# Kernel optimization log

Hardware: AMD Instinct MI355X
Metric: run time of the kernel (lower is better)

The kernel has to match this reference:

```python
import jax, jax.numpy as jnp
import numpy as np

B, T, E, NH, VOCAB, MULT = 1, 1024, 768, 12, 32000, 32
N = E * MULT // NH  # 2048
LN_EPS = 1e-5


def setup_inputs() -> dict:
    key = jax.random.key(0)
    ks = jax.random.split(key, 6)
    return {
        "idx": jax.random.randint(ks[0], (B, T), 0, VOCAB),
        "embed": jax.random.normal(ks[1], (VOCAB, E), jnp.float32) * 0.02,
        "encoder": jax.random.normal(ks[2], (NH, E, N), jnp.float32) * 0.02,
        "encoder_v": jax.random.normal(ks[3], (NH, E, N), jnp.float32) * 0.02,
        "decoder": jax.random.normal(ks[4], (NH * N, E), jnp.float32) * 0.02,
        "lm_head": jax.random.normal(ks[5], (VOCAB, E), jnp.float32) * 0.02,
        "ln_w": jnp.ones((E,), jnp.float32),
        "ln_b": jnp.zeros((E,), jnp.float32),
        "n_layer": 6,
    }


def reference(idx, embed, encoder, encoder_v, decoder, lm_head, ln_w, ln_b, n_layer):
    nh, e, n = encoder.shape
    t = idx.shape[1]
    dec = decoder.reshape(nh, n, e)  # flatten order (h, n) -> h*N + n

    def ln(x):
        m = jnp.mean(x, axis=-1, keepdims=True)
        v = jnp.mean(jnp.square(x - m), axis=-1, keepdims=True)
        return (x - m) * jax.lax.rsqrt(v + LN_EPS) * ln_w + ln_b

    causal = jnp.tril(jnp.ones((t, t), bool))  # [T, T]
    scale = 1.0 / np.sqrt(n).astype(np.float32)

    x = ln(embed[idx])  # [B, T, E]  (the unsqueezed head dim broadcasts; keep it squeezed)
    for _ in range(n_layer):
        # encoder projection + ReLU: [B,T,E] x [H,E,N] -> [B,H,T,N]
        x_sparse = jax.nn.relu(jnp.einsum("bte,hen->bhtn", x, encoder))
        # hand-rolled causal attention, Q=K=x_sparse, V=x (broadcast over heads)
        scores = jnp.einsum("bhqn,bhkn->bhqk", x_sparse, x_sparse) * scale
        scores = jnp.where(causal, scores, -jnp.inf)
        attn = jax.nn.softmax(scores, axis=-1)
        y = jnp.einsum("bhqk,bke->bhqe", attn, x)  # [B,H,T,E]
        y = ln(y)
        y_sparse = jax.nn.relu(jnp.einsum("bhte,hen->bhtn", y, encoder_v))
        xy = x_sparse * y_sparse  # [B,H,T,N]; dropout p=0 -> identity
        y_mlp = jnp.einsum("bhtn,hne->bte", xy, dec)  # decoder matmul
        x = ln(x + ln(y_mlp))
    logits = jnp.einsum("bte,ve->btv", x, lm_head)
    return logits
```

## Files before the change

kernel.cpp:

```cpp
#include <hip/hip_runtime.h>

typedef unsigned short u16;
typedef short bf16x8 __attribute__((ext_vector_type(8)));
typedef float f32x4 __attribute__((ext_vector_type(4)));
typedef u16 u16x4 __attribute__((ext_vector_type(4)));

#define TT     1024
#define EE     768
#define NHH    12
#define ND     2048
#define VOC    32000
#define HNN    24576
#define NLAYER 6
#define LN_EPS 1e-5f

__device__ __forceinline__ float b2f(u16 u){
  unsigned int x = ((unsigned int)u) << 16; float f; __builtin_memcpy(&f, &x, 4); return f;
}
__device__ __forceinline__ u16 f2b(float f){
  unsigned int x; __builtin_memcpy(&x, &f, 4);
  x = x + 0x7fffu + ((x >> 16) & 1u);
  return (u16)(x >> 16);
}

__device__ __forceinline__ void gload16(const void* g, void* lds){
  __builtin_amdgcn_global_load_lds(
      (const __attribute__((address_space(1))) unsigned int*)g,
      (__attribute__((address_space(3))) unsigned int*)(unsigned int)(unsigned long long)lds,
      16, 0, 0);
}

__device__ __forceinline__ bf16x8 ldsr(unsigned addr){
  bf16x8 r;
  asm volatile("ds_read_b128 %0, %1" : "=v"(r) : "v"(addr));
  return r;
}

__device__ __forceinline__ void blk_sum2(float& a, float& b){
  #pragma unroll
  for (int o = 32; o > 0; o >>= 1){ a += __shfl_down(a, o); b += __shfl_down(b, o); }
  __shared__ float sa[4], sb[4];
  int lane = threadIdx.x & 63, wid = threadIdx.x >> 6;
  __syncthreads();
  if (lane == 0){ sa[wid] = a; sb[wid] = b; }
  __syncthreads();
  a = (sa[0] + sa[1]) + (sa[2] + sa[3]);
  b = (sb[0] + sb[1]) + (sb[2] + sb[3]);
}
__device__ __forceinline__ float blk_max(float v){
  #pragma unroll
  for (int o = 32; o > 0; o >>= 1) v = fmaxf(v, __shfl_down(v, o));
  __shared__ float sm[4];
  int lane = threadIdx.x & 63, wid = threadIdx.x >> 6;
  __syncthreads();
  if (lane == 0) sm[wid] = v;
  __syncthreads();
  return fmaxf(fmaxf(sm[0], sm[1]), fmaxf(sm[2], sm[3]));
}
__device__ __forceinline__ float blk_sum(float v){
  #pragma unroll
  for (int o = 32; o > 0; o >>= 1) v += __shfl_down(v, o);
  __shared__ float ss[4];
  int lane = threadIdx.x & 63, wid = threadIdx.x >> 6;
  __syncthreads();
  if (lane == 0) ss[wid] = v;
  __syncthreads();
  return (ss[0] + ss[1]) + (ss[2] + ss[3]);
}

__global__ void transpose_f2b(const float* __restrict__ in, long sIn,
                              u16* __restrict__ out, long sOut, int R, int Cc){
  __shared__ float tile[32][33];
  int z = blockIdx.z;
  in  += (long)z * sIn;
  out += (long)z * sOut;
  int c0 = blockIdx.x * 32, r0 = blockIdx.y * 32;
  int lx = threadIdx.x & 31, ly = threadIdx.x >> 5;
  #pragma unroll
  for (int i = 0; i < 32; i += 8)
    tile[ly + i][lx] = in[(long)(r0 + ly + i) * Cc + (c0 + lx)];
  __syncthreads();
  #pragma unroll
  for (int i = 0; i < 32; i += 8)
    out[(long)(c0 + ly + i) * R + (r0 + lx)] = f2b(tile[lx][ly + i]);
}

__global__ void conv_f2b(const float* __restrict__ in, u16* __restrict__ out){
  long i = ((long)blockIdx.x * 256 + threadIdx.x) * 4;
  float4 v = *(const float4*)(in + i);
  u16x4 o; o.x = f2b(v.x); o.y = f2b(v.y); o.z = f2b(v.z); o.w = f2b(v.w);
  *(u16x4*)(out + i) = o;
}

__global__ void embed_ln(const int* __restrict__ idx, const float* __restrict__ emb,
                         const float* __restrict__ w, const float* __restrict__ b,
                         float* __restrict__ xf, u16* __restrict__ xb, u16* __restrict__ xT){
  int t = blockIdx.x, tid = threadIdx.x;
  const float* src = emb + (long)idx[t] * EE;
  float v[3];
  #pragma unroll
  for (int j = 0; j < 3; j++) v[j] = src[tid + j * 256];
  float s = v[0] + v[1] + v[2];
  float s2 = v[0]*v[0] + v[1]*v[1] + v[2]*v[2];
  blk_sum2(s, s2);
  float m  = s * (1.0f / EE);
  float var = s2 * (1.0f / EE) - m * m;
  float rs = rsqrtf(var + LN_EPS);
  #pragma unroll
  for (int j = 0; j < 3; j++){
    int e = tid + j * 256;
    float o = (v[j] - m) * rs * w[e] + b[e];
    xf[(long)t * EE + e] = o;
    u16 ob = f2b(o);
    xb[(long)t * EE + e] = ob;
    xT[(long)e * TT + t] = ob;
  }
}

__global__ void ln_rows(const float* __restrict__ in, u16* __restrict__ out,
                        const float* __restrict__ w, const float* __restrict__ b){
  long row = blockIdx.x; int tid = threadIdx.x;
  const float* src = in + row * EE;
  float v[3];
  #pragma unroll
  for (int j = 0; j < 3; j++) v[j] = src[tid + j * 256];
  float s = v[0] + v[1] + v[2];
  float s2 = v[0]*v[0] + v[1]*v[1] + v[2]*v[2];
  blk_sum2(s, s2);
  float m = s * (1.0f / EE);
  float var = s2 * (1.0f / EE) - m * m;
  float rs = rsqrtf(var + LN_EPS);
  #pragma unroll
  for (int j = 0; j < 3; j++){
    int e = tid + j * 256;
    out[row * EE + e] = f2b((v[j] - m) * rs * w[e] + b[e]);
  }
}

__global__ void softmax_rows(const float* __restrict__ scores, u16* __restrict__ attn){
  int q = blockIdx.x, h = blockIdx.y, tid = threadIdx.x;
  const float* srow = scores + ((long)h * TT + q) * TT;
  u16* arow = attn + ((long)h * TT + q) * TT;
  float4 v = *(const float4*)(srow + tid * 4);
  float mx = blk_max(fmaxf(fmaxf(v.x, v.y), fmaxf(v.z, v.w)));
  float e0 = __expf(v.x - mx), e1 = __expf(v.y - mx);
  float e2 = __expf(v.z - mx), e3 = __expf(v.w - mx);
  float inv = 1.0f / blk_sum(e0 + e1 + e2 + e3);
  u16x4 o; o.x = f2b(e0 * inv); o.y = f2b(e1 * inv); o.z = f2b(e2 * inv); o.w = f2b(e3 * inv);
  *(u16x4*)(arow + tid * 4) = o;
}

__global__ void residual_ln(const float* __restrict__ part, const float* __restrict__ xin,
                            float* __restrict__ xf, u16* __restrict__ xb, u16* __restrict__ xT,
                            const float* __restrict__ w, const float* __restrict__ b){
  int t = blockIdx.x, tid = threadIdx.x;
  float g[3];
  #pragma unroll
  for (int j = 0; j < 3; j++){
    int e = tid + j * 256;
    float s = 0.f;
    #pragma unroll
    for (int pp = 0; pp < 8; pp++) s += part[((long)pp * TT + t) * EE + e];
    g[j] = s;
  }
  float s = g[0] + g[1] + g[2], s2 = g[0]*g[0] + g[1]*g[1] + g[2]*g[2];
  blk_sum2(s, s2);
  float m = s * (1.0f / EE), var = s2 * (1.0f / EE) - m * m;
  float rs = rsqrtf(var + LN_EPS);
  float hh[3];
  #pragma unroll
  for (int j = 0; j < 3; j++){
    int e = tid + j * 256;
    hh[j] = xin[(long)t * EE + e] + ((g[j] - m) * rs * w[e] + b[e]);
  }
  s = hh[0] + hh[1] + hh[2]; s2 = hh[0]*hh[0] + hh[1]*hh[1] + hh[2]*hh[2];
  blk_sum2(s, s2);
  m = s * (1.0f / EE); var = s2 * (1.0f / EE) - m * m; rs = rsqrtf(var + LN_EPS);
  #pragma unroll
  for (int j = 0; j < 3; j++){
    int e = tid + j * 256;
    float o = (hh[j] - m) * rs * w[e] + b[e];
    xf[(long)t * EE + e] = o;
    u16 ob = f2b(o);
    xb[(long)t * EE + e] = ob;
    xT[(long)e * TT + t] = ob;
  }
}

template<int BM, int BN, int WM, int WN, int DEPTH, int EPI>
__global__ __launch_bounds__(WM*WN*64, 2)
void gemm_pipe(const u16* __restrict__ Ab, long sA,
               const u16* __restrict__ Bb, long sB,
               void* __restrict__ Cb, long sC,
               int grid_m, int grid_mn,
               int K, int lda, int ldb, int ldc, float scale,
               const u16* __restrict__ Mul, long sMul, int ldmul){
  constexpr int THREADS = WM*WN*64;
  constexpr int WMR = BM/WM, WNR = BN/WN;
  constexpr int MI = WMR/16, NI = WNR/16;
  constexpr int BUF  = (BM+BN)*32;
  constexpr int BUFB = BUF*2;
  constexpr int NBUF = DEPTH+1;
  constexpr int AIT = (BM*4)/THREADS, BIT = (BN*4)/THREADS;
  __shared__ __align__(16) u16 S[NBUF*BUF];

  const int nwg = gridDim.x;
  const int orig = blockIdx.x;
  const int q = nwg >> 3, r = nwg & 7;
  const int xcd = orig & 7;
  const int wgid = (xcd < r ? xcd*(q+1) : r*(q+1) + (xcd - r)*q) + (orig >> 3);
  const int z   = wgid / grid_mn;
  const int rem = wgid - z*grid_mn;
  const int nb  = rem / grid_m;
  const int mb  = rem - nb*grid_m;
  const int m0 = mb*BM, n0 = nb*BN;
  const int tid = threadIdx.x, lane = tid & 63, wid = tid >> 6;

  if (EPI == 2 && n0 > m0 + (BM - 1)){
    float* C = (float*)Cb + (long)z * sC;
    constexpr int FIT = (BM*BN)/(THREADS*4);
    #pragma unroll
    for (int i = 0; i < FIT; i++){
      int idx4 = (tid + i*THREADS)*4;
      int rr = idx4 / BN, cc = idx4 - rr*BN;
      *(float4*)&C[(long)(m0+rr)*ldc + n0 + cc] = make_float4(-1e30f,-1e30f,-1e30f,-1e30f);
    }
    return;
  }

  const u16* A = Ab + (long)z*sA;
  const u16* B = Bb + (long)z*sB;

  const int rS = tid >> 2;
  const int cS = (((tid & 3) ^ ((rS >> 1) & 3)) << 3);
  const u16* gA[AIT]; const u16* gB[BIT];
  #pragma unroll
  for (int i = 0; i < AIT; i++) gA[i] = A + (long)(m0 + rS + i*(THREADS/4))*lda + cS;
  #pragma unroll
  for (int i = 0; i < BIT; i++) gB[i] = B + (long)(n0 + rS + i*(THREADS/4))*ldb + cS;

  auto stage = [&](int kt, int buf){
    const int tb = buf*BUF;
    const int ko = kt << 5;
    #pragma unroll
    for (int i = 0; i < AIT; i++)
      gload16(gA[i] + ko, (void*)&S[tb + (i*THREADS + wid*64)*8]);
    #pragma unroll
    for (int i = 0; i < BIT; i++)
      gload16(gB[i] + ko, (void*)&S[tb + BM*32 + (i*THREADS + wid*64)*8]);
  };

  const int wr = wid / WN, wc = wid - wr*WN;
  const int fr = lane & 15, fk = lane >> 4;
  const unsigned ldsBase = (unsigned)(unsigned long long)&S[0];
  unsigned aAd[MI], bAd[NI];
  #pragma unroll
  for (int mi = 0; mi < MI; mi++){
    int rowm = wr*WMR + mi*16 + fr;
    aAd[mi] = ldsBase + (unsigned)(rowm*32 + ((fk ^ ((rowm >> 1) & 3)) << 3)) * 2u;
  }
  #pragma unroll
  for (int ni = 0; ni < NI; ni++){
    int rown = wc*WNR + ni*16 + fr;
    bAd[ni] = ldsBase + (unsigned)(BM*32 + rown*32 + ((fk ^ ((rown >> 1) & 3)) << 3)) * 2u;
  }

  f32x4 acc[MI][NI] = {};

  #pragma unroll
  for (int d = 0; d < DEPTH; d++) stage(d, d);
  if constexpr (DEPTH == 3) asm volatile("s_waitcnt vmcnt(8)" ::: "memory");
  else                      asm volatile("s_waitcnt vmcnt(4)" ::: "memory");
  __builtin_amdgcn_s_barrier();
  __builtin_amdgcn_sched_barrier(0);

  const int NT = K >> 5;
  int rb = 0, wb = DEPTH % NBUF;
  for (int t = 0; t < NT; t++){
    int nx = t + DEPTH; nx = nx < NT ? nx : NT - 1;
    stage(nx, wb);
    const unsigned rbB = (unsigned)rb * BUFB;
    bf16x8 bfr[NI], afr[MI];
    #pragma unroll
    for (int ni = 0; ni < NI; ni++) bfr[ni] = ldsr(bAd[ni] + rbB);
    #pragma unroll
    for (int mi = 0; mi < MI; mi++) afr[mi] = ldsr(aAd[mi] + rbB);
    asm volatile("s_waitcnt lgkmcnt(0)" ::: "memory");
    __builtin_amdgcn_sched_barrier(0);
    __builtin_amdgcn_s_setprio(1);
    #pragma unroll
    for (int mi = 0; mi < MI; mi++)
      #pragma unroll
      for (int ni = 0; ni < NI; ni++)
        acc[mi][ni] = __builtin_amdgcn_mfma_f32_16x16x32_bf16(afr[mi], bfr[ni], acc[mi][ni], 0, 0, 0);
    __builtin_amdgcn_s_setprio(0);
    __builtin_amdgcn_sched_barrier(0);
    if constexpr (DEPTH == 3) asm volatile("s_waitcnt vmcnt(8)" ::: "memory");
    else                      asm volatile("s_waitcnt vmcnt(4)" ::: "memory");
    __builtin_amdgcn_s_barrier();
    __builtin_amdgcn_sched_barrier(0);
    rb = (rb + 1 == NBUF) ? 0 : rb + 1;
    wb = (wb + 1 == NBUF) ? 0 : wb + 1;
  }

  const int er = (lane >> 4) * 4, ec = lane & 15;
  #pragma unroll
  for (int mi = 0; mi < MI; mi++){
    #pragma unroll
    for (int ni = 0; ni < NI; ni++){
      #pragma unroll
      for (int j = 0; j < 4; j++){
        int row = m0 + wr*WMR + mi*16 + er + j;
        int col = n0 + wc*WNR + ni*16 + ec;
        float v = acc[mi][ni][j];
        if (EPI == 0){
          ((float*)Cb + (long)z * sC)[(long)row * ldc + col] = v;
        } else if (EPI == 1){
          v = v > 0.f ? v : 0.f;
          ((u16*)Cb + (long)z * sC)[(long)row * ldc + col] = f2b(v);
        } else if (EPI == 2){
          v *= scale;
          if (col > row) v = -1e30f;
          ((float*)Cb + (long)z * sC)[(long)row * ldc + col] = v;
        } else {
          v = v > 0.f ? v : 0.f;
          float mfv = b2f((Mul + (long)z * sMul)[(long)row * ldmul + col]);
          ((u16*)Cb + (long)z * sC)[(long)row * ldc + col] = f2b(v * mfv);
        }
      }
    }
  }
  asm volatile("s_waitcnt vmcnt(0)" ::: "memory");
}

extern "C" void kernel_launch(void* const* d_in, const int* in_sizes, int n_in,
                              void* d_out, int out_size, void* d_ws, size_t ws_size,
                              hipStream_t stream){
  (void)in_sizes; (void)n_in; (void)out_size; (void)ws_size;
  const int*   idx     = (const int*)  d_in[0];
  const float* embed   = (const float*)d_in[1];
  const float* encoder = (const float*)d_in[2];
  const float* encv    = (const float*)d_in[3];
  const float* decoder = (const float*)d_in[4];
  const float* lm_head = (const float*)d_in[5];
  const float* ln_w    = (const float*)d_in[6];
  const float* ln_b    = (const float*)d_in[7];
  float* out = (float*)d_out;

  char* p = (char*)d_ws;
  auto take = [&](size_t n){ char* r = p; p += (n + 255) & ~(size_t)255; return r; };
  u16*   encT  = (u16*)  take((size_t)NHH * ND * EE * 2);
  u16*   encvT = (u16*)  take((size_t)NHH * ND * EE * 2);
  u16*   decT  = (u16*)  take((size_t)EE * HNN * 2);
  u16*   lmhB  = (u16*)  take((size_t)VOC * EE * 2);
  float* xf    = (float*)take((size_t)TT * EE * 4);
  u16*   xb    = (u16*)  take((size_t)TT * EE * 2);
  u16*   xT    = (u16*)  take((size_t)EE * TT * 2);
  u16*   xs    = (u16*)  take((size_t)NHH * TT * ND * 2);
  char*  big   =         take((size_t)NHH * TT * TT * 4);
  u16*   attn  = (u16*)  take((size_t)NHH * TT * TT * 2);
  u16*   yb    = (u16*)  take((size_t)NHH * TT * EE * 2);
  float* part  = (float*)take((size_t)8 * TT * EE * 4);
  float* scores = (float*)big;
  float* yf     = (float*)big;
  u16*   xy     = (u16*)big;

  dim3 blk(256, 1, 1);

  transpose_f2b<<<dim3(ND / 32, EE / 32, NHH), blk, 0, stream>>>(encoder, (long)EE * ND, encT,  (long)ND * EE, EE, ND);
  transpose_f2b<<<dim3(ND / 32, EE / 32, NHH), blk, 0, stream>>>(encv,    (long)EE * ND, encvT, (long)ND * EE, EE, ND);
  transpose_f2b<<<dim3(EE / 32, HNN / 32, 1),  blk, 0, stream>>>(decoder, 0, decT, 0, HNN, EE);
  conv_f2b<<<dim3((VOC * EE) / 1024, 1, 1), blk, 0, stream>>>(lm_head, lmhB);

  embed_ln<<<dim3(TT, 1, 1), blk, 0, stream>>>(idx, embed, ln_w, ln_b, xf, xb, xT);

  const float scl = 0.022097086912079608f;

  for (int L = 0; L < NLAYER; ++L){
    gemm_pipe<256,256,2,4,3,1><<<dim3(4*8*NHH), dim3(512), 0, stream>>>(
        xb, 0, encT, (long)ND * EE, xs, (long)TT * ND,
        4, 32, EE, EE, EE, ND, 0.f, (const u16*)0, 0, 0);
    gemm_pipe<256,256,2,4,3,2><<<dim3(4*4*NHH), dim3(512), 0, stream>>>(
        xs, (long)TT * ND, xs, (long)TT * ND, scores, (long)TT * TT,
        4, 16, ND, ND, ND, TT, scl, (const u16*)0, 0, 0);
    softmax_rows<<<dim3(TT, NHH, 1), blk, 0, stream>>>(scores, attn);
    gemm_pipe<128,128,2,2,2,0><<<dim3(8*6*NHH), dim3(256), 0, stream>>>(
        attn, (long)TT * TT, xT, 0, yf, (long)TT * EE,
        8, 48, TT, TT, TT, EE, 0.f, (const u16*)0, 0, 0);
    ln_rows<<<dim3(NHH * TT, 1, 1), blk, 0, stream>>>(yf, yb, ln_w, ln_b);
    gemm_pipe<256,256,2,4,3,3><<<dim3(4*8*NHH), dim3(512), 0, stream>>>(
        yb, (long)TT * EE, encvT, (long)ND * EE, xy, (long)ND,
        4, 32, EE, EE, EE, HNN, 0.f, xs, (long)TT * ND, ND);
    gemm_pipe<128,128,2,2,2,0><<<dim3(8*6*8), dim3(256), 0, stream>>>(
        xy, (long)3072, decT, (long)3072, part, (long)TT * EE,
        8, 48, 3072, HNN, HNN, EE, 0.f, (const u16*)0, 0, 0);
    residual_ln<<<dim3(TT, 1, 1), blk, 0, stream>>>(part, xf, xf, xb, xT, ln_w, ln_b);
  }

  gemm_pipe<256,256,2,4,3,0><<<dim3(4*125), dim3(512), 0, stream>>>(
      xb, 0, lmhB, 0, out, 0,
      4, 500, EE, EE, EE, VOC, 0.f, (const u16*)0, 0, 0);
}
```

Baseline: 2.099 ms.

## Add dedicated 128x128 triple-buffered GEMM with causal K-range truncation

Introduces a specialized 128x128 bf16 MFMA GEMM kernel with XCD-aware block remapping, swizzled LDS, three-stage global-to-LDS pipelining and split LDS reads overlapped with MFMA issue. For the attention-times-V GEMM it limits the K loop to the causal prefix (up to the diagonal tile), skipping the masked upper-triangle work. The decoder GEMM also uses the new kernel. It relies on attn being exactly zero beyond the diagonal and adds a second GEMM code path to maintain.

```diff
diff --git a/kernel.cpp b/kernel.cpp
--- a/kernel.cpp
+++ b/kernel.cpp
@@ -333,6 +333,128 @@
   asm volatile("s_waitcnt vmcnt(0)" ::: "memory");
 }
 
+template<bool CAUSAL>
+__global__ __launch_bounds__(256)
+void gemm128(const u16* __restrict__ Ab, long sA,
+             const u16* __restrict__ Bb, long sB,
+             float* __restrict__ Cb, long sC,
+             int grid_m, int grid_mn,
+             int K, int lda, int ldb, int ldc){
+  constexpr unsigned BUFB = 32768u;
+  __shared__ __align__(16) u16 S[3 * 16384];
+
+  const int nwg = gridDim.x, orig = blockIdx.x;
+  const int q = nwg >> 3, r = nwg & 7, xcd = orig & 7;
+  const int wgid = (xcd < r ? xcd*(q+1) : r*(q+1) + (xcd - r)*q) + (orig >> 3);
+  const int z   = wgid / grid_mn;
+  const int rem = wgid - z*grid_mn;
+  const int nb  = rem / grid_m;
+  const int mb  = rem - nb*grid_m;
+  const int m0 = mb*128, n0 = nb*128;
+  const int tid = threadIdx.x, lane = tid & 63, wid = tid >> 6;
+
+  const u16* A = Ab + (long)z*sA;
+  const u16* B = Bb + (long)z*sB;
+
+  const int rS = tid >> 3;
+  const int cS = ((tid & 7) ^ (rS & 7)) << 3;
+  const u16* gA[4]; const u16* gB[4];
+  #pragma unroll
+  for (int i = 0; i < 4; i++) gA[i] = A + (long)(m0 + i*32 + rS)*lda + cS;
+  #pragma unroll
+  for (int i = 0; i < 4; i++) gB[i] = B + (long)(n0 + i*32 + rS)*ldb + cS;
+
+  char* Sb = (char*)&S[0];
+  auto stage = [&](int kt, unsigned bufB){
+    const int ko = kt << 6;
+    #pragma unroll
+    for (int i = 0; i < 4; i++)
+      gload16(gA[i] + ko, Sb + bufB + i*4096 + wid*1024);
+    #pragma unroll
+    for (int i = 0; i < 4; i++)
+      gload16(gB[i] + ko, Sb + bufB + 16384 + i*4096 + wid*1024);
+  };
+
+  const int wr = wid >> 1, wc = wid & 1;
+  const int fr = lane & 15, fk = lane >> 4;
+  const unsigned base = (unsigned)(unsigned long long)Sb;
+  unsigned aAd[2][4], bAd[2][4];
+  #pragma unroll
+  for (int mi = 0; mi < 4; mi++){
+    int row = wr*64 + mi*16 + fr;
+    aAd[0][mi] = base + (unsigned)(row*128 + ((fk ^ (row & 7)) << 4));
+    aAd[1][mi] = base + (unsigned)(row*128 + (((fk + 4) ^ (row & 7)) << 4));
+  }
+  #pragma unroll
+  for (int ni = 0; ni < 4; ni++){
+    int row = wc*64 + ni*16 + fr;
+    bAd[0][ni] = base + 16384u + (unsigned)(row*128 + ((fk ^ (row & 7)) << 4));
+    bAd[1][ni] = base + 16384u + (unsigned)(row*128 + (((fk + 4) ^ (row & 7)) << 4));
+  }
+
+  f32x4 acc[4][4] = {};
+
+  const int NTfull = K >> 6;
+  const int NT = CAUSAL ? ((m0 >> 6) + 2 < NTfull ? (m0 >> 6) + 2 : NTfull) : NTfull;
+
+  stage(0, 0);
+  stage(1, BUFB);
+  stage(NT - 1 < 2 ? NT - 1 : 2, 2u*BUFB);
+  asm volatile("s_waitcnt vmcnt(16)" ::: "memory");
+  __builtin_amdgcn_s_barrier();
+  __builtin_amdgcn_sched_barrier(0);
+
+  unsigned rbB = 0;
+  for (int t = 0; t < NT; t++){
+    bf16x8 a0[4], b0[4], a1[4], b1[4];
+    #pragma unroll
+    for (int ni = 0; ni < 4; ni++) b0[ni] = ldsr(bAd[0][ni] + rbB);
+    #pragma unroll
+    for (int mi = 0; mi < 4; mi++) a0[mi] = ldsr(aAd[0][mi] + rbB);
+    #pragma unroll
+    for (int ni = 0; ni < 4; ni++) b1[ni] = ldsr(bAd[1][ni] + rbB);
+    #pragma unroll
+    for (int mi = 0; mi < 4; mi++) a1[mi] = ldsr(aAd[1][mi] + rbB);
+    asm volatile("s_waitcnt lgkmcnt(8)" ::: "memory");
+    __builtin_amdgcn_sched_barrier(0);
+    __builtin_amdgcn_s_setprio(1);
+    #pragma unroll
+    for (int mi = 0; mi < 4; mi++)
+      #pragma unroll
+      for (int ni = 0; ni < 4; ni++)
+        acc[mi][ni] = __builtin_amdgcn_mfma_f32_16x16x32_bf16(a0[mi], b0[ni], acc[mi][ni], 0, 0, 0);
+    __builtin_amdgcn_s_setprio(0);
+    asm volatile("s_waitcnt lgkmcnt(0)" ::: "memory");
+    __builtin_amdgcn_sched_barrier(0);
+    __builtin_amdgcn_s_setprio(1);
+    #pragma unroll
+    for (int mi = 0; mi < 4; mi++)
+      #pragma unroll
+      for (int ni = 0; ni < 4; ni++)
+        acc[mi][ni] = __builtin_amdgcn_mfma_f32_16x16x32_bf16(a1[mi], b1[ni], acc[mi][ni], 0, 0, 0);
+    __builtin_amdgcn_s_setprio(0);
+    __builtin_amdgcn_sched_barrier(0);
+    __builtin_amdgcn_s_barrier();
+    int nx = t + 3; nx = nx < NT ? nx : NT - 1;
+    stage(nx, rbB);
+    asm volatile("s_waitcnt vmcnt(16)" ::: "memory");
+    __builtin_amdgcn_s_barrier();
+    __builtin_amdgcn_sched_barrier(0);
+    rbB += BUFB; if (rbB == 3u*BUFB) rbB = 0;
+  }
+
+  const int er = (lane >> 4) * 4, ec = lane & 15;
+  float* C = Cb + (long)z*sC;
+  #pragma unroll
+  for (int mi = 0; mi < 4; mi++)
+    #pragma unroll
+    for (int ni = 0; ni < 4; ni++)
+      #pragma unroll
+      for (int j = 0; j < 4; j++)
+        C[(long)(m0 + wr*64 + mi*16 + er + j)*ldc + (n0 + wc*64 + ni*16 + ec)] = acc[mi][ni][j];
+  asm volatile("s_waitcnt vmcnt(0)" ::: "memory");
+}
+
 extern "C" void kernel_launch(void* const* d_in, const int* in_sizes, int n_in,
                               void* d_out, int out_size, void* d_ws, size_t ws_size,
                               hipStream_t stream){
@@ -384,16 +506,16 @@
         xs, (long)TT * ND, xs, (long)TT * ND, scores, (long)TT * TT,
         4, 16, ND, ND, ND, TT, scl, (const u16*)0, 0, 0);
     softmax_rows<<<dim3(TT, NHH, 1), blk, 0, stream>>>(scores, attn);
-    gemm_pipe<128,128,2,2,2,0><<<dim3(8*6*NHH), dim3(256), 0, stream>>>(
+    gemm128<true><<<dim3(8*6*NHH), blk, 0, stream>>>(
         attn, (long)TT * TT, xT, 0, yf, (long)TT * EE,
-        8, 48, TT, TT, TT, EE, 0.f, (const u16*)0, 0, 0);
+        8, 48, TT, TT, TT, EE);
     ln_rows<<<dim3(NHH * TT, 1, 1), blk, 0, stream>>>(yf, yb, ln_w, ln_b);
     gemm_pipe<256,256,2,4,3,3><<<dim3(4*8*NHH), dim3(512), 0, stream>>>(
         yb, (long)TT * EE, encvT, (long)ND * EE, xy, (long)ND,
         4, 32, EE, EE, EE, HNN, 0.f, xs, (long)TT * ND, ND);
-    gemm_pipe<128,128,2,2,2,0><<<dim3(8*6*8), dim3(256), 0, stream>>>(
+    gemm128<false><<<dim3(8*6*8), blk, 0, stream>>>(
         xy, (long)3072, decT, (long)3072, part, (long)TT * EE,
-        8, 48, 3072, HNN, HNN, EE, 0.f, (const u16*)0, 0, 0);
+        8, 48, 3072, HNN, HNN, EE);
     residual_ln<<<dim3(TT, 1, 1), blk, 0, stream>>>(part, xf, xf, xb, xT, ln_w, ln_b);
   }
 
```

Result: no change. 2.105 ms (+0.3%).

## Add simple split-K GEMM with causal K-skip for attn@V and decoder

Applied to the files above, without the earlier changes.

Adds a new 128x128 single-buffer MFMA GEMM kernel. It replaces the attn@x GEMM, where the causal variant stops the K loop at the diagonal block to skip zeroed attention columns. It also replaces the decoder GEMM, raising split-K from 8 to 16 partitions and reusing the attention buffer for partial sums. The aim is to cut wasted work past the causal mask and improve occupancy in the decoder. The trade-off is a simpler non-pipelined kernel with larger partial-sum traffic in the residual reduction.

```diff
diff --git a/kernel.cpp b/kernel.cpp
--- a/kernel.cpp
+++ b/kernel.cpp
@@ -13,6 +13,7 @@
 #define HNN    24576
 #define NLAYER 6
 #define LN_EPS 1e-5f
+#define SPLITK 16
 
 __device__ __forceinline__ float b2f(u16 u){
   unsigned int x = ((unsigned int)u) << 16; float f; __builtin_memcpy(&f, &x, 4); return f;
@@ -150,6 +151,7 @@
   *(u16x4*)(arow + tid * 4) = o;
 }
 
+template<int P>
 __global__ void residual_ln(const float* __restrict__ part, const float* __restrict__ xin,
                             float* __restrict__ xf, u16* __restrict__ xb, u16* __restrict__ xT,
                             const float* __restrict__ w, const float* __restrict__ b){
@@ -160,7 +162,7 @@
     int e = tid + j * 256;
     float s = 0.f;
     #pragma unroll
-    for (int pp = 0; pp < 8; pp++) s += part[((long)pp * TT + t) * EE + e];
+    for (int pp = 0; pp < P; pp++) s += part[((long)pp * TT + t) * EE + e];
     g[j] = s;
   }
   float s = g[0] + g[1] + g[2], s2 = g[0]*g[0] + g[1]*g[1] + g[2]*g[2];
@@ -333,6 +335,69 @@
   asm volatile("s_waitcnt vmcnt(0)" ::: "memory");
 }
 
+template<bool CAUSAL>
+__global__ __launch_bounds__(256)
+void gemm_sk(const u16* __restrict__ Ab, long sA,
+             const u16* __restrict__ Bb, long sB,
+             float* __restrict__ Cb, long sC,
+             int grid_m, int grid_mn,
+             int K, int lda, int ldb, int ldc){
+  __shared__ u16 As[128 * 32];
+  __shared__ u16 Bs[128 * 32];
+  const int nwg = gridDim.x, orig = blockIdx.x;
+  const int q = nwg >> 3, r = nwg & 7, xcd = orig & 7;
+  const int wgid = (xcd < r ? xcd*(q+1) : r*(q+1) + (xcd - r)*q) + (orig >> 3);
+  const int z   = wgid / grid_mn;
+  const int rem = wgid - z*grid_mn;
+  const int nb  = rem / grid_m;
+  const int mb  = rem - nb*grid_m;
+  const int m0 = mb*128, n0 = nb*128;
+  const int tid = threadIdx.x, lane = tid & 63, wid = tid >> 6;
+
+  const u16* A = Ab + (long)z*sA;
+  const u16* B = Bb + (long)z*sB;
+
+  f32x4 acc[4][4] = {};
+  const int wr = wid >> 1, wc = wid & 1;
+  const int fr = lane & 15, fk = lane >> 4;
+  const int Keff = CAUSAL ? (m0 + 128 < K ? m0 + 128 : K) : K;
+
+  const u16* ga = A + (long)(m0 + wid * 32 + (lane >> 2)) * lda + (lane & 3) * 8;
+  const u16* gb = B + (long)(n0 + wid * 32 + (lane >> 2)) * ldb + (lane & 3) * 8;
+
+  for (int k0 = 0; k0 < Keff; k0 += 32){
+    gload16(ga + k0,            (void*)&As[(wid * 32) * 32]);
+    gload16(ga + k0 + 16 * lda, (void*)&As[(wid * 32 + 16) * 32]);
+    gload16(gb + k0,            (void*)&Bs[(wid * 32) * 32]);
+    gload16(gb + k0 + 16 * ldb, (void*)&Bs[(wid * 32 + 16) * 32]);
+    asm volatile("s_waitcnt vmcnt(0)" ::: "memory");
+    __syncthreads();
+    bf16x8 af[4], bfv[4];
+    #pragma unroll
+    for (int mi = 0; mi < 4; mi++)
+      af[mi] = *(const bf16x8*)&As[(wr * 64 + mi * 16 + fr) * 32 + fk * 8];
+    #pragma unroll
+    for (int ni = 0; ni < 4; ni++)
+      bfv[ni] = *(const bf16x8*)&Bs[(wc * 64 + ni * 16 + fr) * 32 + fk * 8];
+    #pragma unroll
+    for (int mi = 0; mi < 4; mi++)
+      #pragma unroll
+      for (int ni = 0; ni < 4; ni++)
+        acc[mi][ni] = __builtin_amdgcn_mfma_f32_16x16x32_bf16(af[mi], bfv[ni], acc[mi][ni], 0, 0, 0);
+    __syncthreads();
+  }
+
+  const int er = (lane >> 4) * 4, ec = lane & 15;
+  float* C = Cb + (long)z*sC;
+  #pragma unroll
+  for (int mi = 0; mi < 4; mi++)
+    #pragma unroll
+    for (int ni = 0; ni < 4; ni++)
+      #pragma unroll
+      for (int j = 0; j < 4; j++)
+        C[(long)(m0 + wr*64 + mi*16 + er + j)*ldc + (n0 + wc*64 + ni*16 + ec)] = acc[mi][ni][j];
+}
+
 extern "C" void kernel_launch(void* const* d_in, const int* in_sizes, int n_in,
                               void* d_out, int out_size, void* d_ws, size_t ws_size,
                               hipStream_t stream){
@@ -360,10 +425,11 @@
   char*  big   =         take((size_t)NHH * TT * TT * 4);
   u16*   attn  = (u16*)  take((size_t)NHH * TT * TT * 2);
   u16*   yb    = (u16*)  take((size_t)NHH * TT * EE * 2);
-  float* part  = (float*)take((size_t)8 * TT * EE * 4);
+  take((size_t)8 * TT * EE * 4);
   float* scores = (float*)big;
   float* yf     = (float*)big;
   u16*   xy     = (u16*)big;
+  float* part   = (float*)attn;
 
   dim3 blk(256, 1, 1);
 
@@ -384,17 +450,17 @@
         xs, (long)TT * ND, xs, (long)TT * ND, scores, (long)TT * TT,
         4, 16, ND, ND, ND, TT, scl, (const u16*)0, 0, 0);
     softmax_rows<<<dim3(TT, NHH, 1), blk, 0, stream>>>(scores, attn);
-    gemm_pipe<128,128,2,2,2,0><<<dim3(8*6*NHH), dim3(256), 0, stream>>>(
+    gemm_sk<true><<<dim3(8*6*NHH), blk, 0, stream>>>(
         attn, (long)TT * TT, xT, 0, yf, (long)TT * EE,
-        8, 48, TT, TT, TT, EE, 0.f, (const u16*)0, 0, 0);
+        8, 48, TT, TT, TT, EE);
     ln_rows<<<dim3(NHH * TT, 1, 1), blk, 0, stream>>>(yf, yb, ln_w, ln_b);
     gemm_pipe<256,256,2,4,3,3><<<dim3(4*8*NHH), dim3(512), 0, stream>>>(
         yb, (long)TT * EE, encvT, (long)ND * EE, xy, (long)ND,
         4, 32, EE, EE, EE, HNN, 0.f, xs, (long)TT * ND, ND);
-    gemm_pipe<128,128,2,2,2,0><<<dim3(8*6*8), dim3(256), 0, stream>>>(
-        xy, (long)3072, decT, (long)3072, part, (long)TT * EE,
-        8, 48, 3072, HNN, HNN, EE, 0.f, (const u16*)0, 0, 0);
-    residual_ln<<<dim3(TT, 1, 1), blk, 0, stream>>>(part, xf, xf, xb, xT, ln_w, ln_b);
+    gemm_sk<false><<<dim3(8*6*SPLITK), blk, 0, stream>>>(
+        xy, (long)(HNN / SPLITK), decT, (long)(HNN / SPLITK), part, (long)TT * EE,
+        8, 48, HNN / SPLITK, HNN, HNN, EE);
+    residual_ln<SPLITK><<<dim3(TT, 1, 1), blk, 0, stream>>>(part, xf, xf, xb, xT, ln_w, ln_b);
   }
 
   gemm_pipe<256,256,2,4,3,0><<<dim3(4*125), dim3(512), 0, stream>>>(
```

New measurement: 2.076 ms. Within noise of the previous version (-1.1%).

## Rewrite GEMM pipeline with split A/B staging, causal K clamp, and deeper split-K

Applied to the files above, without the earlier changes.

Replaces the generic multi-depth GEMM with a triple-buffered kernel. Each K step is split into two half-phases that interleave the A and B global-to-LDS loads with MFMA work, and the LDS swizzle changes to a 64-byte row layout. The attention-times-V GEMM now clamps K to the causal extent of each row block, so it skips the all-zero upper-triangle tiles. The decoder GEMM goes from split-K 8 to 16 for more workgroups, with partials stored in the attn buffer and reduced by residual_ln. The extra barriers per K step and the doubled partial-sum traffic are the added costs.

```diff
diff --git a/kernel.cpp b/kernel.cpp
--- a/kernel.cpp
+++ b/kernel.cpp
@@ -13,6 +13,7 @@
 #define HNN    24576
 #define NLAYER 6
 #define LN_EPS 1e-5f
+#define SPLITK 16
 
 __device__ __forceinline__ float b2f(u16 u){
   unsigned int x = ((unsigned int)u) << 16; float f; __builtin_memcpy(&f, &x, 4); return f;
@@ -150,6 +151,7 @@
   *(u16x4*)(arow + tid * 4) = o;
 }
 
+template<int P>
 __global__ void residual_ln(const float* __restrict__ part, const float* __restrict__ xin,
                             float* __restrict__ xf, u16* __restrict__ xb, u16* __restrict__ xT,
                             const float* __restrict__ w, const float* __restrict__ b){
@@ -160,7 +162,7 @@
     int e = tid + j * 256;
     float s = 0.f;
     #pragma unroll
-    for (int pp = 0; pp < 8; pp++) s += part[((long)pp * TT + t) * EE + e];
+    for (int pp = 0; pp < P; pp++) s += part[((long)pp * TT + t) * EE + e];
     g[j] = s;
   }
   float s = g[0] + g[1] + g[2], s2 = g[0]*g[0] + g[1]*g[1] + g[2]*g[2];
@@ -187,27 +189,25 @@
   }
 }
 
-template<int BM, int BN, int WM, int WN, int DEPTH, int EPI>
-__global__ __launch_bounds__(WM*WN*64, 2)
-void gemm_pipe(const u16* __restrict__ Ab, long sA,
-               const u16* __restrict__ Bb, long sB,
-               void* __restrict__ Cb, long sC,
-               int grid_m, int grid_mn,
-               int K, int lda, int ldb, int ldc, float scale,
-               const u16* __restrict__ Mul, long sMul, int ldmul){
+template<int BM, int WM, int WN, int EPI, bool CCLAMP>
+__global__ __launch_bounds__(WM*WN*64, (WM*WN*64 == 512) ? 2 : 3)
+void gemm8p(const u16* __restrict__ Ab, long sA,
+            const u16* __restrict__ Bb, long sB,
+            void* __restrict__ Cb, long sC,
+            int grid_m, int grid_mn,
+            int K, int lda, int ldb, int ldc, float scale,
+            const u16* __restrict__ Mul, long sMul, int ldmul){
+  constexpr int BN = BM;
   constexpr int THREADS = WM*WN*64;
   constexpr int WMR = BM/WM, WNR = BN/WN;
-  constexpr int MI = WMR/16, NI = WNR/16;
-  constexpr int BUF  = (BM+BN)*32;
-  constexpr int BUFB = BUF*2;
-  constexpr int NBUF = DEPTH+1;
-  constexpr int AIT = (BM*4)/THREADS, BIT = (BN*4)/THREADS;
-  __shared__ __align__(16) u16 S[NBUF*BUF];
-
-  const int nwg = gridDim.x;
-  const int orig = blockIdx.x;
-  const int q = nwg >> 3, r = nwg & 7;
-  const int xcd = orig & 7;
+  constexpr int MI = WMR/16, NI = WNR/16, MH = MI/2;
+  constexpr unsigned BUFB   = (unsigned)(BM+BN)*64u;
+  constexpr int      ROWS_RD = THREADS/4;
+  constexpr unsigned ISSUE_B = (unsigned)THREADS*16u;
+  __shared__ __align__(16) u16 S[3*BUFB/2];
+
+  const int nwg = gridDim.x, orig = blockIdx.x;
+  const int q = nwg >> 3, r = nwg & 7, xcd = orig & 7;
   const int wgid = (xcd < r ? xcd*(q+1) : r*(q+1) + (xcd - r)*q) + (orig >> 3);
   const int z   = wgid / grid_mn;
   const int rem = wgid - z*grid_mn;
@@ -232,76 +232,95 @@
   const u16* B = Bb + (long)z*sB;
 
   const int rS = tid >> 2;
-  const int cS = (((tid & 3) ^ ((rS >> 1) & 3)) << 3);
-  const u16* gA[AIT]; const u16* gB[BIT];
-  #pragma unroll
-  for (int i = 0; i < AIT; i++) gA[i] = A + (long)(m0 + rS + i*(THREADS/4))*lda + cS;
-  #pragma unroll
-  for (int i = 0; i < BIT; i++) gB[i] = B + (long)(n0 + rS + i*(THREADS/4))*ldb + cS;
-
-  auto stage = [&](int kt, int buf){
-    const int tb = buf*BUF;
+  const int cS = (((tid & 3) ^ (rS & 3)) << 3);
+  const u16* gA[2]; const u16* gB[2];
+  #pragma unroll
+  for (int i = 0; i < 2; i++) gA[i] = A + (long)(m0 + i*ROWS_RD + rS)*lda + cS;
+  #pragma unroll
+  for (int i = 0; i < 2; i++) gB[i] = B + (long)(n0 + i*ROWS_RD + rS)*ldb + cS;
+
+  char* Sb = (char*)&S[0];
+  auto stageA = [&](int kt, unsigned bB){
     const int ko = kt << 5;
-    #pragma unroll
-    for (int i = 0; i < AIT; i++)
-      gload16(gA[i] + ko, (void*)&S[tb + (i*THREADS + wid*64)*8]);
-    #pragma unroll
-    for (int i = 0; i < BIT; i++)
-      gload16(gB[i] + ko, (void*)&S[tb + BM*32 + (i*THREADS + wid*64)*8]);
+    gload16(gA[0] + ko, Sb + bB + wid*1024u);
+    gload16(gA[1] + ko, Sb + bB + ISSUE_B + wid*1024u);
   };
-
-  const int wr = wid / WN, wc = wid - wr*WN;
+  auto stageB = [&](int kt, unsigned bB){
+    const int ko = kt << 5;
+    gload16(gB[0] + ko, Sb + bB + (unsigned)BM*64u + wid*1024u);
+    gload16(gB[1] + ko, Sb + bB + (unsigned)BM*64u + ISSUE_B + wid*1024u);
+  };
+
+  const int wr = wid / WN, wc = wid % WN;
   const int fr = lane & 15, fk = lane >> 4;
-  const unsigned ldsBase = (unsigned)(unsigned long long)&S[0];
+  const unsigned base = (unsigned)(unsigned long long)Sb;
   unsigned aAd[MI], bAd[NI];
   #pragma unroll
   for (int mi = 0; mi < MI; mi++){
-    int rowm = wr*WMR + mi*16 + fr;
-    aAd[mi] = ldsBase + (unsigned)(rowm*32 + ((fk ^ ((rowm >> 1) & 3)) << 3)) * 2u;
+    int row = wr*WMR + mi*16 + fr;
+    aAd[mi] = base + (unsigned)(row*64 + ((fk ^ (row & 3)) << 4));
   }
   #pragma unroll
   for (int ni = 0; ni < NI; ni++){
-    int rown = wc*WNR + ni*16 + fr;
-    bAd[ni] = ldsBase + (unsigned)(BM*32 + rown*32 + ((fk ^ ((rown >> 1) & 3)) << 3)) * 2u;
-  }
+    int row = wc*WNR + ni*16 + fr;
+    bAd[ni] = base + (unsigned)BM*64u + (unsigned)(row*64 + ((fk ^ (row & 3)) << 4));
+  }
+
+  const int Keff = CCLAMP ? (m0 + BM < K ? m0 + BM : K) : K;
+  const int NT = Keff >> 5;
 
   f32x4 acc[MI][NI] = {};
 
-  #pragma unroll
-  for (int d = 0; d < DEPTH; d++) stage(d, d);
-  if constexpr (DEPTH == 3) asm volatile("s_waitcnt vmcnt(8)" ::: "memory");
-  else                      asm volatile("s_waitcnt vmcnt(4)" ::: "memory");
+  stageA(0, 0); stageB(0, 0);
+  stageA(1, BUFB); stageB(1, BUFB);
+  asm volatile("s_waitcnt vmcnt(4)" ::: "memory");
   __builtin_amdgcn_s_barrier();
   __builtin_amdgcn_sched_barrier(0);
 
-  const int NT = K >> 5;
-  int rb = 0, wb = DEPTH % NBUF;
+  unsigned rb = 0, wb = 2;
   for (int t = 0; t < NT; t++){
-    int nx = t + DEPTH; nx = nx < NT ? nx : NT - 1;
-    stage(nx, wb);
-    const unsigned rbB = (unsigned)rb * BUFB;
-    bf16x8 bfr[NI], afr[MI];
+    const unsigned rbB = rb*BUFB, wbB = wb*BUFB;
+    const int nx = (t + 2 < NT) ? t + 2 : NT - 1;
+    bf16x8 bfr[NI], afr[MH];
     #pragma unroll
     for (int ni = 0; ni < NI; ni++) bfr[ni] = ldsr(bAd[ni] + rbB);
     #pragma unroll
-    for (int mi = 0; mi < MI; mi++) afr[mi] = ldsr(aAd[mi] + rbB);
+    for (int u = 0; u < MH; u++)    afr[u]  = ldsr(aAd[u] + rbB);
+    stageA(nx, wbB);
+    __builtin_amdgcn_s_barrier();
     asm volatile("s_waitcnt lgkmcnt(0)" ::: "memory");
     __builtin_amdgcn_sched_barrier(0);
     __builtin_amdgcn_s_setprio(1);
     #pragma unroll
-    for (int mi = 0; mi < MI; mi++)
+    for (int u = 0; u < MH; u++)
       #pragma unroll
       for (int ni = 0; ni < NI; ni++)
-        acc[mi][ni] = __builtin_amdgcn_mfma_f32_16x16x32_bf16(afr[mi], bfr[ni], acc[mi][ni], 0, 0, 0);
+        acc[u][ni] = __builtin_amdgcn_mfma_f32_16x16x32_bf16(afr[u], bfr[ni], acc[u][ni], 0, 0, 0);
     __builtin_amdgcn_s_setprio(0);
-    __builtin_amdgcn_sched_barrier(0);
-    if constexpr (DEPTH == 3) asm volatile("s_waitcnt vmcnt(8)" ::: "memory");
-    else                      asm volatile("s_waitcnt vmcnt(4)" ::: "memory");
+    asm volatile("s_waitcnt vmcnt(4)" ::: "memory");
     __builtin_amdgcn_s_barrier();
     __builtin_amdgcn_sched_barrier(0);
-    rb = (rb + 1 == NBUF) ? 0 : rb + 1;
-    wb = (wb + 1 == NBUF) ? 0 : wb + 1;
-  }
+    bf16x8 afr2[MH];
+    #pragma unroll
+    for (int u = 0; u < MH; u++) afr2[u] = ldsr(aAd[MH + u] + rbB);
+    stageB(nx, wbB);
+    __builtin_amdgcn_s_barrier();
+    asm volatile("s_waitcnt lgkmcnt(0)" ::: "memory");
+    __builtin_amdgcn_sched_barrier(0);
+    __builtin_amdgcn_s_setprio(1);
+    #pragma unroll
+    for (int u = 0; u < MH; u++)
+      #pragma unroll
+      for (int ni = 0; ni < NI; ni++)
+        acc[MH+u][ni] = __builtin_amdgcn_mfma_f32_16x16x32_bf16(afr2[u], bfr[ni], acc[MH+u][ni], 0, 0, 0);
+    __builtin_amdgcn_s_setprio(0);
+    asm volatile("s_waitcnt vmcnt(4)" ::: "memory");
+    __builtin_amdgcn_s_barrier();
+    __builtin_amdgcn_sched_barrier(0);
+    rb = (rb + 1 == 3) ? 0 : rb + 1;
+    wb = (wb + 1 == 3) ? 0 : wb + 1;
+  }
+  asm volatile("s_waitcnt vmcnt(0)" ::: "memory");
 
   const int er = (lane >> 4) * 4, ec = lane & 15;
   #pragma unroll
@@ -330,7 +349,6 @@
       }
     }
   }
-  asm volatile("s_waitcnt vmcnt(0)" ::: "memory");
 }
 
 extern "C" void kernel_launch(void* const* d_in, const int* in_sizes, int n_in,
@@ -360,10 +378,11 @@
   char*  big   =         take((size_t)NHH * TT * TT * 4);
   u16*   attn  = (u16*)  take((size_t)NHH * TT * TT * 2);
   u16*   yb    = (u16*)  take((size_t)NHH * TT * EE * 2);
-  float* part  = (float*)take((size_t)8 * TT * EE * 4);
+  take((size_t)8 * TT * EE * 4);
   float* scores = (float*)big;
   float* yf     = (float*)big;
   u16*   xy     = (u16*)big;
+  float* part   = (float*)attn;
 
   dim3 blk(256, 1, 1);
 
@@ -377,27 +396,27 @@
   const float scl = 0.022097086912079608f;
 
   for (int L = 0; L < NLAYER; ++L){
-    gemm_pipe<256,256,2,4,3,1><<<dim3(4*8*NHH), dim3(512), 0, stream>>>(
+    gemm8p<256,2,4,1,false><<<dim3(4*8*NHH), dim3(512), 0, stream>>>(
         xb, 0, encT, (long)ND * EE, xs, (long)TT * ND,
         4, 32, EE, EE, EE, ND, 0.f, (const u16*)0, 0, 0);
-    gemm_pipe<256,256,2,4,3,2><<<dim3(4*4*NHH), dim3(512), 0, stream>>>(
+    gemm8p<256,2,4,2,false><<<dim3(4*4*NHH), dim3(512), 0, stream>>>(
         xs, (long)TT * ND, xs, (long)TT * ND, scores, (long)TT * TT,
         4, 16, ND, ND, ND, TT, scl, (const u16*)0, 0, 0);
     softmax_rows<<<dim3(TT, NHH, 1), blk, 0, stream>>>(scores, attn);
-    gemm_pipe<128,128,2,2,2,0><<<dim3(8*6*NHH), dim3(256), 0, stream>>>(
+    gemm8p<128,2,2,0,true><<<dim3(8*6*NHH), blk, 0, stream>>>(
         attn, (long)TT * TT, xT, 0, yf, (long)TT * EE,
         8, 48, TT, TT, TT, EE, 0.f, (const u16*)0, 0, 0);
     ln_rows<<<dim3(NHH * TT, 1, 1), blk, 0, stream>>>(yf, yb, ln_w, ln_b);
-    gemm_pipe<256,256,2,4,3,3><<<dim3(4*8*NHH), dim3(512), 0, stream>>>(
+    gemm8p<256,2,4,3,false><<<dim3(4*8*NHH), dim3(512), 0, stream>>>(
         yb, (long)TT * EE, encvT, (long)ND * EE, xy, (long)ND,
         4, 32, EE, EE, EE, HNN, 0.f, xs, (long)TT * ND, ND);
-    gemm_pipe<128,128,2,2,2,0><<<dim3(8*6*8), dim3(256), 0, stream>>>(
-        xy, (long)3072, decT, (long)3072, part, (long)TT * EE,
-        8, 48, 3072, HNN, HNN, EE, 0.f, (const u16*)0, 0, 0);
-    residual_ln<<<dim3(TT, 1, 1), blk, 0, stream>>>(part, xf, xf, xb, xT, ln_w, ln_b);
-  }
-
-  gemm_pipe<256,256,2,4,3,0><<<dim3(4*125), dim3(512), 0, stream>>>(
+    gemm8p<128,2,2,0,false><<<dim3(8*6*SPLITK), blk, 0, stream>>>(
+        xy, (long)(HNN / SPLITK), decT, (long)(HNN / SPLITK), part, (long)TT * EE,
+        8, 48, HNN / SPLITK, HNN, HNN, EE, 0.f, (const u16*)0, 0, 0);
+    residual_ln<SPLITK><<<dim3(TT, 1, 1), blk, 0, stream>>>(part, xf, xf, xb, xT, ln_w, ln_b);
+  }
+
+  gemm8p<256,2,4,0,false><<<dim3(4*125), dim3(512), 0, stream>>>(
       xb, 0, lmhB, 0, out, 0,
       4, 500, EE, EE, EE, VOC, 0.f, (const u16*)0, 0, 0);
 }
```

After: 1.996 ms. -4.9%, faster.
